# Kernel optimization log

Measured on AMD Instinct MI355X. Metric: run time of the kernel, lower is better.

## Reference

```python
import jax, jax.numpy as jnp
import numpy as np

KERNEL_MUL = 2.0
KERNEL_NUM = 5


def setup_inputs() -> dict:
    key = jax.random.key(0)
    k1, k2 = jax.random.split(key)
    N, D = 8192, 256
    subggroup = jax.random.randint(k1, (N, 1), 0, 2, dtype=jnp.int64)
    outputs = jax.random.normal(k2, (N, D), dtype=jnp.float32)
    return {"subggroup": subggroup, "outputs": outputs}


def reference(subggroup, outputs):
    # Binary labels: rows with label 0 form `source` (Min), label 1 form `target` (Maj).
    # concat(source, target) is a permutation of `outputs`, so we compute the
    # full NxN multi-RBF kernel once and take masked means -- identical math.
    sub = subggroup[:, 0]
    m0 = (sub == 0).astype(outputs.dtype)  # source mask
    m1 = (sub == 1).astype(outputs.dtype)  # target mask
    n = outputs.shape[0]

    # Pairwise squared L2 distances via matmul (fused cdist), [N, N]
    sq = jnp.sum(outputs * outputs, axis=-1)
    L2 = jnp.maximum(sq[:, None] + sq[None, :] - 2.0 * (outputs @ outputs.T), 0.0)

    # bandwidth computed from detached distances (torch uses L2_distance.data)
    bandwidth = jax.lax.stop_gradient(jnp.sum(L2)) / (n * n - n)
    bandwidth = bandwidth / (KERNEL_MUL ** (KERNEL_NUM // 2))

    K = jnp.zeros_like(L2)
    for i in range(KERNEL_NUM):
        K = K + jnp.exp(-L2 / (bandwidth * (KERNEL_MUL ** i)))

    n0 = jnp.sum(m0)
    n1 = jnp.sum(m1)
    XX = jnp.einsum('i,ij,j->', m0, K, m0) / (n0 * n0)
    YY = jnp.einsum('i,ij,j->', m1, K, m1) / (n1 * n1)
    XY = jnp.einsum('i,ij,j->', m0, K, m1) / (n0 * n1)
    YX = jnp.einsum('i,ij,j->', m1, K, m0) / (n1 * n0)
    return XX + YY - XY - YX
```

## Files before the change

### kernel.cpp

```cpp
#include <hip/hip_runtime.h>

#define N_ROWS 8192
#define DIMS   256
#define NTILE  64
#define NFULL  1024
#define NCHUNK 1056
#define K1B    256
#define K3B    512

typedef _Float16 f16x4 __attribute__((ext_vector_type(4)));
typedef _Float16 f16x8 __attribute__((ext_vector_type(8)));
typedef float   f32x16 __attribute__((ext_vector_type(16)));

#define WS_PLANE  0
#define WS_SQ     (4 * 1024 * 1024)
#define WS_RED    (WS_SQ + 32768)
#define WS_SSQA   (WS_RED + 1024)
#define WS_N0A    (WS_SSQA + 4)
#define WS_SC     (WS_N0A + 4)
#define WS_PART   (WS_RED + 2048)

struct Scalars {
    unsigned int ctr;
    unsigned int t3;
};

#define BL(dst, p, o) asm volatile("global_load_dwordx4 %0, %1, off offset:" o \
                                   : "=v"(dst) : "v"(p))

__global__ __launch_bounds__(256) void k1_rows(const float* __restrict__ x,
                                               const long long* __restrict__ sub,
                                               float* __restrict__ sq,
                                               float* __restrict__ colsumA,
                                               float* __restrict__ ssqA,
                                               unsigned int* __restrict__ n0A,
                                               unsigned short* __restrict__ plane) {
    __shared__ _Float16 stg[16 * 512];
    __shared__ float cls[4][256];
    __shared__ float smq[4];
    const int t = threadIdx.x;
    const int l = t & 63;
    const int w = t >> 6;
    const int base = blockIdx.x * 32;

    float4 colacc = make_float4(0.f, 0.f, 0.f, 0.f);
    float  my_sumsq = 0.f;

    const int ks  = l >> 2;
    const int shi = ((l >> 1) & 1) * 32;
    const int j4  = (l & 1) * 4;

    #pragma unroll
    for (int r = 0; r < 8; ++r) {
        const int rr  = w * 8 + r;
        const int row = base + rr;
        const float4 v = ((const float4*)(x + (size_t)row * DIMS))[l];
        colacc.x += v.x; colacc.y += v.y; colacc.z += v.z; colacc.w += v.w;

        f16x4 h = { (_Float16)v.x, (_Float16)v.y, (_Float16)v.z, (_Float16)v.w };
        *(f16x4*)&stg[ks * 512 + (rr + shi) * 8 + j4] = h;

        float s = v.x * v.x + v.y * v.y + v.z * v.z + v.w * v.w;
        #pragma unroll
        for (int off = 32; off; off >>= 1) s += __shfl_down(s, off, 64);
        if (l == 0) { sq[row] = s; my_sumsq += s; }
    }
    if (l == 0) smq[w] = my_sumsq;
    *(float4*)&cls[w][l * 4] = colacc;
    __syncthreads();

    {
        const uint4* src = (const uint4*)stg;
        uint4* dst = (uint4*)(plane + (size_t)blockIdx.x * 8192);
        #pragma unroll
        for (int i = 0; i < 4; ++i) dst[i * 256 + t] = src[i * 256 + t];
    }

    atomicAdd(&colsumA[t], cls[0][t] + cls[1][t] + cls[2][t] + cls[3][t]);
    if (t == 0) atomicAdd(ssqA, smq[0] + smq[1] + smq[2] + smq[3]);
    if (w == 1) {
        unsigned long long m1 = __ballot(l < 32 && (int)sub[base + l] == 0);
        if (l == 0) atomicAdd(n0A, (unsigned int)__popcll(m1));
    }
}

__global__ __launch_bounds__(256, 2) void k3_mmd(const unsigned short* __restrict__ plane,
                                                 const long long* __restrict__ sub,
                                                 const float* __restrict__ sq,
                                                 const float* __restrict__ colsumA,
                                                 const float* __restrict__ ssqA,
                                                 const unsigned int* __restrict__ n0A,
                                                 Scalars* sc,
                                                 double* __restrict__ partial,
                                                 float* __restrict__ out) {
    __shared__ char ldsA[65536];
    __shared__ float2 sqwI[128];
    __shared__ double dd[4];
    __shared__ unsigned int qb;

    const int t  = threadIdx.x;
    const int l  = t & 63;
    const int w  = t >> 6;
    const int lh = l >> 5;
    const int ln = l & 31;

    float c2, w0, w1;
    {
        const float4 c4 = ((const float4*)colsumA)[l];
        float cs2 = c4.x * c4.x + c4.y * c4.y + c4.z * c4.z + c4.w * c4.w;
        #pragma unroll
        for (int off = 32; off; off >>= 1) cs2 += __shfl_xor(cs2, off, 64);
        const float ssq = *ssqA;
        const float n0f = (float)*n0A;
        const double n = (double)N_ROWS;
        const double sumL2 = 2.0 * n * (double)ssq - 2.0 * (double)cs2;
        const double bw = sumL2 / (n * n - n) / 4.0;
        c2 = (float)(-1.4426950408889634 / (16.0 * bw));
        const double n0 = (double)n0f, n1 = n - n0;
        w0 = (float)( 1.0 / n0);
        w1 = (float)(-1.0 / n1);
    }

    double dsum = 0.0;
    f16x8 b[16];

    if (t == 0) qb = atomicAdd(&sc->ctr, 1u);
    for (;;) {
        __syncthreads();
        const unsigned q0 = qb;
        if (q0 >= NCHUNK) break;
        int bi, bj, nt;
        if (q0 < NFULL) {
            int q = (int)q0; bi = 0;
            while (q >= ((NTILE - bi) >> 1)) { q -= (NTILE - bi) >> 1; ++bi; }
            bj = bi + q * 2;
            nt = 2;
        } else {
            bi = 2 * (int)(q0 - NFULL) + 1;
            bj = NTILE - 1;
            nt = 1;
        }

        #pragma unroll
        for (int i = 0; i < 16; ++i) {
            const unsigned short* g = plane + (((size_t)(bi * 4 + w) * 16 + i) << 9) + (l << 3);
            char* lp = ldsA + ((w * 16 + i) << 10);
            __builtin_amdgcn_global_load_lds(
                (const __attribute__((address_space(1))) unsigned int*)(const void*)g,
                (__attribute__((address_space(3))) unsigned int*)(void*)lp, 16, 0, 0);
        }
        if (t < 128) {
            const int I = bi * 128 + t;
            sqwI[t] = make_float2(sq[I], ((int)sub[I] == 0) ? w0 : w1);
        }
        {
            const unsigned short* p0 = plane + (((size_t)(bj * 4 + w) * 16) << 9) + (l << 3);
            const unsigned short* p1 = p0 + 2048;
            const unsigned short* p2 = p0 + 4096;
            const unsigned short* p3 = p0 + 6144;
            BL(b[0], p0,"0"); BL(b[1], p0,"1024"); BL(b[2], p0,"2048"); BL(b[3], p0,"3072");
            BL(b[4], p1,"0"); BL(b[5], p1,"1024"); BL(b[6], p1,"2048"); BL(b[7], p1,"3072");
            BL(b[8], p2,"0"); BL(b[9], p2,"1024"); BL(b[10],p2,"2048"); BL(b[11],p2,"3072");
            BL(b[12],p3,"0"); BL(b[13],p3,"1024"); BL(b[14],p3,"2048"); BL(b[15],p3,"3072");
        }
        const int J0 = bj * 128 + w * 32 + ln;
        float sJ  = sq[J0];
        float wJv = ((int)sub[J0] == 0) ? w0 : w1;
        __syncthreads();

        for (int tt = 0; tt < nt; ++tt, ++bj) {
            const bool dg = (bj == bi);
            asm volatile("s_waitcnt vmcnt(0)" ::: "memory");
            __builtin_amdgcn_sched_barrier(0);

            f32x16 acc[4] = {};
            f16x8 a0, a1, a2, a3, x0, x1, x2, x3;
            a0 = *(const f16x8*)(ldsA + (( 0 * 16 + 0) << 10) + (l << 4));
            a1 = *(const f16x8*)(ldsA + (( 1 * 16 + 0) << 10) + (l << 4));
            a2 = *(const f16x8*)(ldsA + (( 2 * 16 + 0) << 10) + (l << 4));
            a3 = *(const f16x8*)(ldsA + (( 3 * 16 + 0) << 10) + (l << 4));
            #pragma unroll
            for (int ks = 0; ks < 16; ++ks) {
                if (ks < 15) {
                    x0 = *(const f16x8*)(ldsA + ((0 * 16 + ks + 1) << 10) + (l << 4));
                    x1 = *(const f16x8*)(ldsA + ((1 * 16 + ks + 1) << 10) + (l << 4));
                    x2 = *(const f16x8*)(ldsA + ((2 * 16 + ks + 1) << 10) + (l << 4));
                    x3 = *(const f16x8*)(ldsA + ((3 * 16 + ks + 1) << 10) + (l << 4));
                }
                acc[0] = __builtin_amdgcn_mfma_f32_32x32x16_f16(a0, b[ks], acc[0], 0, 0, 0);
                acc[1] = __builtin_amdgcn_mfma_f32_32x32x16_f16(a1, b[ks], acc[1], 0, 0, 0);
                acc[2] = __builtin_amdgcn_mfma_f32_32x32x16_f16(a2, b[ks], acc[2], 0, 0, 0);
                acc[3] = __builtin_amdgcn_mfma_f32_32x32x16_f16(a3, b[ks], acc[3], 0, 0, 0);
                a0 = x0; a1 = x1; a2 = x2; a3 = x3;
            }

            if (tt == nt - 1 && t == 0) qb = atomicAdd(&sc->ctr, 1u);

            float sJn = 0.f, wJn = 0.f;
            if (tt + 1 < nt) {
                const unsigned short* p0 = plane + (((size_t)((bj + 1) * 4 + w) * 16) << 9) + (l << 3);
                const unsigned short* p1 = p0 + 2048;
                const unsigned short* p2 = p0 + 4096;
                const unsigned short* p3 = p0 + 6144;
                BL(b[0], p0,"0"); BL(b[1], p0,"1024"); BL(b[2], p0,"2048"); BL(b[3], p0,"3072");
                BL(b[4], p1,"0"); BL(b[5], p1,"1024"); BL(b[6], p1,"2048"); BL(b[7], p1,"3072");
                BL(b[8], p2,"0"); BL(b[9], p2,"1024"); BL(b[10],p2,"2048"); BL(b[11],p2,"3072");
                BL(b[12],p3,"0"); BL(b[13],p3,"1024"); BL(b[14],p3,"2048"); BL(b[15],p3,"3072");
                const int Jn = (bj + 1) * 128 + w * 32 + ln;
                sJn = sq[Jn];
                wJn = ((int)sub[Jn] == 0) ? w0 : w1;
            }

            float part = 0.f;
            #pragma unroll
            for (int m = 0; m < 4; ++m) {
                #pragma unroll
                for (int r = 0; r < 16; ++r) {
                    const int Il = m * 32 + (r & 3) + ((r >> 2) << 3) + (lh << 2);
                    const float2 pi = sqwI[Il];
                    float l2 = fmaxf(pi.x + sJ - 2.f * acc[m][r], 0.f);
                    const float e  = __builtin_amdgcn_exp2f(l2 * c2);
                    const float e2 = e * e, e4 = e2 * e2, e8 = e4 * e4;
                    const float K  = ((e + e2) + (e4 + e8)) + e8 * e8;
                    float w2 = pi.y * wJv;
                    if (dg) {
                        const int Jl = w * 32 + ln;
                        w2 *= (Il < Jl) ? 2.f : ((Il == Jl) ? 1.f : 0.f);
                    }
                    part = fmaf(K, w2, part);
                }
            }
            dsum += (double)part * (dg ? 1.0 : 2.0);
            sJ = sJn; wJv = wJn;
        }
    }

    #pragma unroll
    for (int off = 32; off; off >>= 1) dsum += __shfl_down(dsum, off, 64);
    __syncthreads();
    if (l == 0) dd[w] = dsum;
    __syncthreads();
    if (t == 0) {
        partial[blockIdx.x] = dd[0] + dd[1] + dd[2] + dd[3];
        __threadfence();
        qb = (atomicAdd(&sc->t3, 1u) == K3B - 1) ? 1u : 0u;
    }
    __syncthreads();
    if (qb) {
        __threadfence();
        double v = partial[t] + partial[t + 256];
        #pragma unroll
        for (int off = 32; off; off >>= 1) v += __shfl_down(v, off, 64);
        if (l == 0) dd[w] = v;
        __syncthreads();
        if (t == 0) out[0] = (float)(dd[0] + dd[1] + dd[2] + dd[3]);
    }
}

extern "C" void kernel_launch(void* const* d_in, const int* in_sizes, int n_in,
                              void* d_out, int out_size, void* d_ws, size_t ws_size,
                              hipStream_t stream) {
    const long long* sub = (const long long*)d_in[0];
    const float*     x   = (const float*)d_in[1];
    float* out = (float*)d_out;

    char* ws = (char*)d_ws;
    unsigned short* plane   = (unsigned short*)(ws + WS_PLANE);
    float*          sq      = (float*)(ws + WS_SQ);
    float*          colsumA = (float*)(ws + WS_RED);
    float*          ssqA    = (float*)(ws + WS_SSQA);
    unsigned int*   n0A     = (unsigned int*)(ws + WS_N0A);
    Scalars*        sc      = (Scalars*)(ws + WS_SC);
    double*         partial = (double*)(ws + WS_PART);

    hipMemsetAsync(ws + WS_RED, 0, 1040, stream);
    k1_rows<<<K1B, 256, 0, stream>>>(x, sub, sq, colsumA, ssqA, n0A, plane);
    k3_mmd<<<K3B, 256, 0, stream>>>(plane, sub, sq, colsumA, ssqA, n0A, sc, partial, out);
}
```

Baseline: 115.4 us.

## Prefetch next work chunk's A tile and B registers during exp epilogue

The persistent MMD kernel now fetches the next chunk index and issues the next chunk's A-tile global-to-LDS loads, B-register loads and row norm/weight loads before running the exp/reduction epilogue of the current tile. The sqwI row metadata is double-buffered so the epilogue can keep reading the current chunk's values while the next ones are written. This is meant to hide global load latency at chunk boundaries behind the exp-heavy epilogue. The cost is an extra block-wide barrier per chunk and more live registers and LDS during the epilogue.

```diff
diff --git a/kernel.cpp b/kernel.cpp
--- a/kernel.cpp
+++ b/kernel.cpp
@@ -94,7 +94,7 @@
                                                  double* __restrict__ partial,
                                                  float* __restrict__ out) {
     __shared__ char ldsA[65536];
-    __shared__ float2 sqwI[128];
+    __shared__ float2 sqwI[2][128];
     __shared__ double dd[4];
     __shared__ unsigned int qb;
 
@@ -123,13 +123,9 @@
 
     double dsum = 0.0;
     f16x8 b[16];
-
-    if (t == 0) qb = atomicAdd(&sc->ctr, 1u);
-    for (;;) {
-        __syncthreads();
-        const unsigned q0 = qb;
-        if (q0 >= NCHUNK) break;
-        int bi, bj, nt;
+    float sJ = 0.f, wJv = 0.f;
+
+    auto decode = [](unsigned q0, int& bi, int& bj, int& nt) {
         if (q0 < NFULL) {
             int q = (int)q0; bi = 0;
             while (q >= ((NTILE - bi) >> 1)) { q -= (NTILE - bi) >> 1; ++bi; }
@@ -140,36 +136,53 @@
             bj = NTILE - 1;
             nt = 1;
         }
-
+    };
+    auto stageA = [&](int bi_) {
         #pragma unroll
         for (int i = 0; i < 16; ++i) {
-            const unsigned short* g = plane + (((size_t)(bi * 4 + w) * 16 + i) << 9) + (l << 3);
+            const unsigned short* g = plane + (((size_t)(bi_ * 4 + w) * 16 + i) << 9) + (l << 3);
             char* lp = ldsA + ((w * 16 + i) << 10);
             __builtin_amdgcn_global_load_lds(
                 (const __attribute__((address_space(1))) unsigned int*)(const void*)g,
                 (__attribute__((address_space(3))) unsigned int*)(void*)lp, 16, 0, 0);
         }
+    };
+    auto issueB = [&](int bj_) {
+        const unsigned short* p0 = plane + (((size_t)(bj_ * 4 + w) * 16) << 9) + (l << 3);
+        const unsigned short* p1 = p0 + 2048;
+        const unsigned short* p2 = p0 + 4096;
+        const unsigned short* p3 = p0 + 6144;
+        BL(b[0], p0,"0"); BL(b[1], p0,"1024"); BL(b[2], p0,"2048"); BL(b[3], p0,"3072");
+        BL(b[4], p1,"0"); BL(b[5], p1,"1024"); BL(b[6], p1,"2048"); BL(b[7], p1,"3072");
+        BL(b[8], p2,"0"); BL(b[9], p2,"1024"); BL(b[10],p2,"2048"); BL(b[11],p2,"3072");
+        BL(b[12],p3,"0"); BL(b[13],p3,"1024"); BL(b[14],p3,"2048"); BL(b[15],p3,"3072");
+    };
+
+    if (t == 0) qb = atomicAdd(&sc->ctr, 1u);
+    __syncthreads();
+    unsigned q0 = qb;
+    int bi = 0, bj = 0, nt = 0, cb = 0;
+    if (q0 < NCHUNK) {
+        decode(q0, bi, bj, nt);
+        stageA(bi);
         if (t < 128) {
             const int I = bi * 128 + t;
-            sqwI[t] = make_float2(sq[I], ((int)sub[I] == 0) ? w0 : w1);
+            sqwI[0][t] = make_float2(sq[I], ((int)sub[I] == 0) ? w0 : w1);
         }
-        {
-            const unsigned short* p0 = plane + (((size_t)(bj * 4 + w) * 16) << 9) + (l << 3);
-            const unsigned short* p1 = p0 + 2048;
-            const unsigned short* p2 = p0 + 4096;
-            const unsigned short* p3 = p0 + 6144;
-            BL(b[0], p0,"0"); BL(b[1], p0,"1024"); BL(b[2], p0,"2048"); BL(b[3], p0,"3072");
-            BL(b[4], p1,"0"); BL(b[5], p1,"1024"); BL(b[6], p1,"2048"); BL(b[7], p1,"3072");
-            BL(b[8], p2,"0"); BL(b[9], p2,"1024"); BL(b[10],p2,"2048"); BL(b[11],p2,"3072");
-            BL(b[12],p3,"0"); BL(b[13],p3,"1024"); BL(b[14],p3,"2048"); BL(b[15],p3,"3072");
-        }
+        issueB(bj);
         const int J0 = bj * 128 + w * 32 + ln;
-        float sJ  = sq[J0];
-        float wJv = ((int)sub[J0] == 0) ? w0 : w1;
-        __syncthreads();
-
-        for (int tt = 0; tt < nt; ++tt, ++bj) {
-            const bool dg = (bj == bi);
+        sJ  = sq[J0];
+        wJv = ((int)sub[J0] == 0) ? w0 : w1;
+    }
+    __syncthreads();
+
+    while (q0 < NCHUNK) {
+        unsigned nq = q0;
+        int nbi = bi, nbj = bj, nnt = nt;
+
+        for (int tt = 0; tt < nt; ++tt) {
+            const int bjc = bj + tt;
+            const bool dg = (bjc == bi);
             asm volatile("s_waitcnt vmcnt(0)" ::: "memory");
             __builtin_amdgcn_sched_barrier(0);
 
@@ -194,21 +207,28 @@
                 a0 = x0; a1 = x1; a2 = x2; a3 = x3;
             }
 
-            if (tt == nt - 1 && t == 0) qb = atomicAdd(&sc->ctr, 1u);
-
             float sJn = 0.f, wJn = 0.f;
             if (tt + 1 < nt) {
-                const unsigned short* p0 = plane + (((size_t)((bj + 1) * 4 + w) * 16) << 9) + (l << 3);
-                const unsigned short* p1 = p0 + 2048;
-                const unsigned short* p2 = p0 + 4096;
-                const unsigned short* p3 = p0 + 6144;
-                BL(b[0], p0,"0"); BL(b[1], p0,"1024"); BL(b[2], p0,"2048"); BL(b[3], p0,"3072");
-                BL(b[4], p1,"0"); BL(b[5], p1,"1024"); BL(b[6], p1,"2048"); BL(b[7], p1,"3072");
-                BL(b[8], p2,"0"); BL(b[9], p2,"1024"); BL(b[10],p2,"2048"); BL(b[11],p2,"3072");
-                BL(b[12],p3,"0"); BL(b[13],p3,"1024"); BL(b[14],p3,"2048"); BL(b[15],p3,"3072");
-                const int Jn = (bj + 1) * 128 + w * 32 + ln;
+                issueB(bjc + 1);
+                const int Jn = (bjc + 1) * 128 + w * 32 + ln;
                 sJn = sq[Jn];
                 wJn = ((int)sub[Jn] == 0) ? w0 : w1;
+            } else {
+                if (t == 0) qb = atomicAdd(&sc->ctr, 1u);
+                __syncthreads();
+                nq = qb;
+                if (nq < NCHUNK) {
+                    decode(nq, nbi, nbj, nnt);
+                    stageA(nbi);
+                    if (t < 128) {
+                        const int I = nbi * 128 + t;
+                        sqwI[cb ^ 1][t] = make_float2(sq[I], ((int)sub[I] == 0) ? w0 : w1);
+                    }
+                    issueB(nbj);
+                    const int Jn = nbj * 128 + w * 32 + ln;
+                    sJn = sq[Jn];
+                    wJn = ((int)sub[Jn] == 0) ? w0 : w1;
+                }
             }
 
             float part = 0.f;
@@ -217,7 +237,7 @@
                 #pragma unroll
                 for (int r = 0; r < 16; ++r) {
                     const int Il = m * 32 + (r & 3) + ((r >> 2) << 3) + (lh << 2);
-                    const float2 pi = sqwI[Il];
+                    const float2 pi = sqwI[cb][Il];
                     float l2 = fmaxf(pi.x + sJ - 2.f * acc[m][r], 0.f);
                     const float e  = __builtin_amdgcn_exp2f(l2 * c2);
                     const float e2 = e * e, e4 = e2 * e2, e8 = e4 * e4;
@@ -233,6 +253,9 @@
             dsum += (double)part * (dg ? 1.0 : 2.0);
             sJ = sJn; wJv = wJn;
         }
+
+        __syncthreads();
+        q0 = nq; bi = nbi; bj = nbj; nt = nnt; cb ^= 1;
     }
 
     #pragma unroll
```

New measurement: 117.1 us. Within noise of the previous version (+1.5%).
